# Optimization experiments

Hardware: AMD Instinct MI355X
Metric: run time of the kernel (lower is better)

## Reference

```python
import jax, jax.numpy as jnp
import numpy as np

NEG_INF = -1e30  # safe -inf surrogate to avoid nan in logsumexp


def _ctc_loss_sum(log_probs, labels, input_lengths, label_lengths):
    # log_probs: (T, N, C) already log-softmaxed; blank = 0
    T, N, C = log_probs.shape
    S = labels.shape[1]
    L = 2 * S + 1  # extended label sequence: blank-interleaved

    # extended labels: [blank, y1, blank, y2, ..., blank]
    ext = jnp.zeros((N, L), dtype=jnp.int32).at[:, 1::2].set(labels.astype(jnp.int32))
    # gather emission log-probs for extended labels: (T, N, L)
    lp_ext = jnp.take_along_axis(log_probs, jnp.broadcast_to(ext[None], (T, N, L)), axis=2)

    # transition from l-2 allowed only for non-blank labels differing from ext[l-2]
    ext_m2 = jnp.pad(ext, ((0, 0), (2, 0)), constant_values=-1)[:, :L]
    allow_skip = (ext != 0) & (ext != ext_m2)  # (N, L)

    # alpha at t=0
    alpha0 = jnp.full((N, L), NEG_INF, dtype=log_probs.dtype)
    alpha0 = alpha0.at[:, 0].set(lp_ext[0, :, 0])
    alpha0 = alpha0.at[:, 1].set(jnp.where(label_lengths > 0, lp_ext[0, :, 1], NEG_INF))

    def step(alpha, t_and_lp):
        t, lp_t = t_and_lp  # lp_t: (N, L)
        a1 = jnp.pad(alpha, ((0, 0), (1, 0)), constant_values=NEG_INF)[:, :L]
        a2 = jnp.pad(alpha, ((0, 0), (2, 0)), constant_values=NEG_INF)[:, :L]
        a2 = jnp.where(allow_skip, a2, NEG_INF)
        m = jnp.maximum(jnp.maximum(alpha, a1), a2)
        lse = m + jnp.log(jnp.exp(alpha - m) + jnp.exp(a1 - m) + jnp.exp(a2 - m))
        new = jnp.where(m > NEG_INF / 2, lse + lp_t, NEG_INF)
        # freeze alpha past each sequence's input length
        alpha = jnp.where((t < input_lengths)[:, None], new, alpha)
        return alpha, None

    alpha, _ = jax.lax.scan(step, alpha0, (jnp.arange(1, T), lp_ext[1:]))

    # log-likelihood = logsumexp(alpha[2*Sl], alpha[2*Sl - 1])
    idx = (2 * label_lengths).astype(jnp.int32)
    a_last = jnp.take_along_axis(alpha, idx[:, None], axis=1)[:, 0]
    a_prev = jnp.take_along_axis(alpha, jnp.maximum(idx - 1, 0)[:, None], axis=1)[:, 0]
    a_prev = jnp.where(label_lengths > 0, a_prev, NEG_INF)
    m = jnp.maximum(a_last, a_prev)
    ll = m + jnp.log(jnp.exp(a_last - m) + jnp.exp(a_prev - m))
    loss = -ll
    # zero_infinity=True: replace infinite losses with 0
    loss = jnp.where(loss < -NEG_INF / 2, loss, 0.0)
    return jnp.sum(loss)


def setup_inputs() -> dict:
    T, N, C, S = 512, 32, 4000, 64
    key = jax.random.key(0)
    k1, k2 = jax.random.split(key)
    inputs = jax.random.normal(k1, (T, N, C), dtype=jnp.float32)
    labels = jax.random.randint(k2, (N, S), 1, C, dtype=jnp.int32)  # exclude blank=0
    input_lengths = jnp.full((N,), T, dtype=jnp.int32)
    label_lengths = jnp.full((N,), S, dtype=jnp.int32)
    return {"inputs": inputs, "labels": labels,
            "input_lengths": input_lengths, "label_lengths": label_lengths}


def reference(inputs, labels, input_lengths, label_lengths):
    log_probs = jax.nn.log_softmax(inputs, axis=2)
    return _ctc_loss_sum(log_probs, labels, input_lengths, label_lengths)
```

## Files before the change

kernel.cpp:

```cpp
#include <hip/hip_runtime.h>

#define LN2 0.6931471805599453f

constexpr int T = 512, N = 32, C = 4000, S = 64;
constexpr int TN   = T * N;
constexpr int ROWF = 68;
constexpr int CT   = 16;
constexpr int NC   = T / CT;

__global__ __launch_bounds__(256) void k_softmax_probs(
    const float* __restrict__ x, const int* __restrict__ labels,
    float* __restrict__ pp)
{
    int row  = blockIdx.x * 4 + (threadIdx.x >> 6);
    int lane = threadIdx.x & 63;
    const float*  rp  = x + (size_t)row * C;
    const float4* rp4 = reinterpret_cast<const float4*>(rp);

    float m = -INFINITY, s = 0.f;
    #pragma unroll
    for (int k = 0; k < 15; ++k) {
        float4 v = rp4[lane + 64 * k];
        float mv = fmaxf(fmaxf(v.x, v.y), fmaxf(v.z, v.w));
        float s4 = __expf(v.x - mv) + __expf(v.y - mv) +
                   __expf(v.z - mv) + __expf(v.w - mv);
        float nm = fmaxf(m, mv);
        s = s * __expf(m - nm) + s4 * __expf(mv - nm);
        m = nm;
    }
    if (lane < 40) {
        float4 v = rp4[960 + lane];
        float mv = fmaxf(fmaxf(v.x, v.y), fmaxf(v.z, v.w));
        float s4 = __expf(v.x - mv) + __expf(v.y - mv) +
                   __expf(v.z - mv) + __expf(v.w - mv);
        float nm = fmaxf(m, mv);
        s = s * __expf(m - nm) + s4 * __expf(mv - nm);
        m = nm;
    }
    for (int off = 32; off; off >>= 1) {
        float om = __shfl_xor(m, off), os = __shfl_xor(s, off);
        float nm = fmaxf(m, om);
        s = s * __expf(m - nm) + os * __expf(om - nm);
        m = nm;
    }
    float logZ = m + __logf(s);

    int t = row >> 5, n = row & 31;
    int c = labels[n * S + lane];
    float* outp = pp + ((size_t)n * T + t) * ROWF;
    outp[1 + lane] = __expf(rp[c] - logZ);
    if (lane == 0) outp[0] = __expf(rp[0] - logZ);
}

__device__ __forceinline__ float dpp_shr1_zero(float x) {
    int r = __builtin_amdgcn_update_dpp(0, __float_as_int(x),
                                        0x138 , 0xf, 0xf, false);
    return __int_as_float(r);
}
template <int CTRL>
__device__ __forceinline__ float dpp_max_step(float x) {
    int t = __builtin_amdgcn_update_dpp(__float_as_int(x), __float_as_int(x),
                                        CTRL, 0xf, 0xf, false);
    return fmaxf(x, __int_as_float(t));
}
__device__ __forceinline__ float wave_max_bcast(float x) {
    x = dpp_max_step<0xB1>(x);
    x = dpp_max_step<0x4E>(x);
    x = dpp_max_step<0x141>(x);
    x = dpp_max_step<0x140>(x);
    x = dpp_max_step<0x142>(x);
    x = dpp_max_step<0x143>(x);
    return __int_as_float(__builtin_amdgcn_readlane(__float_as_int(x), 63));
}
__device__ __forceinline__ void renorm_apply(float g, float& a0, float& a1,
                                             float& aX, int& SH, int target) {
    unsigned bits = __float_as_uint(g);
    int k = (bits == 0u) ? 0 : (target - ((int)(bits >> 23) - 127));
    a0 = ldexpf(a0, k); a1 = ldexpf(a1, k); aX = ldexpf(aX, k);
    SH += k;
}

__device__ __forceinline__ void single_step(const float* R, int lane, float skf,
                                            float& a0, float& a1, float& aX) {
    float cb = R[0], cl = R[1 + lane];
    float p1 = dpp_shr1_zero(a1);
    float n0 = (a0 + p1) * cb;
    float n1 = fmaf(skf, p1, a0 + a1) * cl;
    float nX = (aX + a1) * cb;
    a0 = n0; a1 = n1; aX = nX;
}

__device__ __forceinline__ void pair_step(const float* R0, const float* R1,
    int lane, float skf, float skUf, float skk,
    float& a0, float& a1, float& aX)
{
    float cb1 = R0[0], cl1 = R0[1 + lane];
    float cb2 = R1[0], cl2 = R1[1 + lane];
    float clU = dpp_shr1_zero(cl1);
    float W   = clU * cl2;
    float A   = cb1 * cb2;
    float B   = clU * cb2;
    float Cc  = A + B;
    float D   = skUf * B;
    float s1  = cb1 + cl1;
    float E   = s1 * cl2;
    float F   = cl1 * cl2;
    float G   = skf * W;
    float H   = fmaf(skf, F + W, cb1 * cl2);
    float I   = skk * W;
    float Y0  = cl1 * cb2;
    float Y1  = s1 * cb2;
    float Y2  = skf * Y0;
    float p1  = dpp_shr1_zero(a1);
    float p0  = dpp_shr1_zero(a0);
    float p2  = dpp_shr1_zero(p1);
    float n0  = fmaf(p0, B, a0 * A) + fmaf(p2, D, p1 * Cc);
    float n1  = fmaf(a1, F, a0 * E) + fmaf(p2, I, fmaf(p1, H, p0 * G));
    float nX  = fmaf(a1, Y1, aX * A) + fmaf(p1, Y2, a0 * Y0);
    a0 = n0; a1 = n1; aX = nX;
}

__global__ __launch_bounds__(64) void k_ctc_alpha(
    const float* __restrict__ pp, const int* __restrict__ labels,
    const int* __restrict__ input_len, const int* __restrict__ label_len,
    float* __restrict__ loss_out)
{
    __shared__ float lds[2][CT][256];
    const int n = blockIdx.x, lane = threadIdx.x;
    const float* bp = pp + (size_t)n * T * ROWF;
    const int Tin = input_len[n], Sl = label_len[n];

    const int li   = labels[n * S + lane];
    const int lim1 = lane ? labels[n * S + lane - 1] : -1;
    const bool skip_ok = (lane > 0) && (li != 0) && (li != lim1);
    const float skf  = skip_ok ? 1.f : 0.f;
    const float skUf = dpp_shr1_zero(skf);
    const float skk  = skf * skUf;

    asm volatile("s_waitcnt vmcnt(0)" ::: "memory");
    __builtin_amdgcn_sched_barrier(0);

    float a0 = 0.f, a1 = 0.f, aX = 0.f;
    int SH = 0;

#define ISSUE(cc) do {                                                        \
    const float* cp_ = bp + (size_t)(cc) * CT * ROWF;                         \
    _Pragma("unroll")                                                         \
    for (int d_ = 0; d_ < CT; ++d_)                                           \
        __builtin_amdgcn_global_load_lds(cp_ + (size_t)d_ * ROWF + lane * 4,  \
                                         &lds[(cc) & 1][d_][0], 16, 0, 0);    \
    } while (0)

#define WIN4(BUF, D0) do {                                                    \
    float gs_ = fmaxf(fmaxf(a0, a1), aX);                                     \
    pair_step(&lds[BUF][D0    ][0], &lds[BUF][D0 + 1][0], lane, skf, skUf, skk, a0, a1, aX); \
    pair_step(&lds[BUF][D0 + 2][0], &lds[BUF][D0 + 3][0], lane, skf, skUf, skk, a0, a1, aX); \
    pair_step(&lds[BUF][D0 + 4][0], &lds[BUF][D0 + 5][0], lane, skf, skUf, skk, a0, a1, aX); \
    pair_step(&lds[BUF][D0 + 6][0], &lds[BUF][D0 + 7][0], lane, skf, skUf, skk, a0, a1, aX); \
    renorm_apply(wave_max_bcast(gs_), a0, a1, aX, SH, 90);                    \
} while (0)

    ISSUE(0);
    ISSUE(1);

    if (Tin == T) {
        asm volatile("s_waitcnt vmcnt(16)" ::: "memory");
        __builtin_amdgcn_sched_barrier(0);
        a0 = (lane == 0) ? lds[0][0][0] : 0.f;
        a1 = (lane == 0 && Sl > 0) ? lds[0][0][1] : 0.f;
        {
            float gs_ = fmaxf(a0, a1);
            single_step(&lds[0][1][0], lane, skf, a0, a1, aX);
            pair_step(&lds[0][2][0], &lds[0][3][0], lane, skf, skUf, skk, a0, a1, aX);
            pair_step(&lds[0][4][0], &lds[0][5][0], lane, skf, skUf, skk, a0, a1, aX);
            pair_step(&lds[0][6][0], &lds[0][7][0], lane, skf, skUf, skk, a0, a1, aX);
            renorm_apply(wave_max_bcast(gs_), a0, a1, aX, SH, 90);
            WIN4(0, 8);
        }
        __builtin_amdgcn_sched_barrier(0);
        ISSUE(2);
        for (int c = 1; c < NC; ++c) {
            if (c < NC - 1) asm volatile("s_waitcnt vmcnt(16)" ::: "memory");
            else            asm volatile("s_waitcnt vmcnt(0)"  ::: "memory");
            __builtin_amdgcn_sched_barrier(0);
            int buf = c & 1;
            WIN4(buf, 0);
            WIN4(buf, 8);
            if (c + 2 < NC) {
                __builtin_amdgcn_sched_barrier(0);
                ISSUE(c + 2);
            }
        }
    } else {
#define GSTEP(cc, dd) do {                                                    \
    float cb_ = lds[(cc) & 1][dd][0];                                         \
    float cl_ = lds[(cc) & 1][dd][1 + lane];                                  \
    float p1_ = dpp_shr1_zero(a1);                                            \
    float na0_ = (a0 + p1_) * cb_;                                            \
    float na1_ = fmaf(skf, p1_, a0 + a1) * cl_;                               \
    float naX_ = (aX + a1) * cb_;                                             \
    int t_ = (cc) * CT + (dd);                                                \
    bool act_ = (unsigned)(t_ - 1) < (unsigned)(Tin - 1);                     \
    a0 = act_ ? na0_ : a0;                                                    \
    a1 = act_ ? na1_ : a1;                                                    \
    aX = act_ ? naX_ : aX;                                                    \
    if (((dd) & 3) == 3) {                                                    \
        float g_ = wave_max_bcast(fmaxf(a0, fmaxf(a1, aX)));                  \
        renorm_apply(g_, a0, a1, aX, SH, 100);                                \
    }                                                                         \
} while (0)
        asm volatile("s_waitcnt vmcnt(16)" ::: "memory");
        __builtin_amdgcn_sched_barrier(0);
        a0 = (lane == 0) ? lds[0][0][0] : 0.f;
        a1 = (lane == 0 && Sl > 0) ? lds[0][0][1] : 0.f;
        #pragma unroll
        for (int d = 1; d < CT; ++d) GSTEP(0, d);
        __builtin_amdgcn_sched_barrier(0);
        ISSUE(2);
        for (int c = 1; c < NC; ++c) {
            if (c < NC - 1) asm volatile("s_waitcnt vmcnt(16)" ::: "memory");
            else            asm volatile("s_waitcnt vmcnt(0)"  ::: "memory");
            __builtin_amdgcn_sched_barrier(0);
            #pragma unroll
            for (int d = 0; d < CT; ++d) GSTEP(c, d);
            if (c + 2 < NC) {
                __builtin_amdgcn_sched_barrier(0);
                ISSUE(c + 2);
            }
        }
#undef GSTEP
    }
#undef ISSUE
#undef WIN4

    float a_last = (Sl >= S) ? __shfl(aX, 63) : __shfl(a0, Sl);
    float a_prev_raw = __shfl(a1, (Sl > 0) ? (Sl - 1) : 0);
    float a_prev = (Sl > 0) ? a_prev_raw : 0.f;
    if (lane == 0) {
        float sum  = a_last + a_prev;
        float ll2  = log2f(sum) - (float)SH;
        float loss = -ll2 * LN2;
        if (!(loss < 5e29f)) loss = 0.f;
        loss_out[n] = loss;
    }
}

__global__ __launch_bounds__(64) void k_reduce(
    const float* __restrict__ loss, float* __restrict__ out)
{
    int lane = threadIdx.x;
    float v = (lane < N) ? loss[lane] : 0.f;
    for (int off = 32; off; off >>= 1) v += __shfl_xor(v, off);
    if (lane == 0) out[0] = v;
}

extern "C" void kernel_launch(void* const* d_in, const int* in_sizes, int n_in,
                              void* d_out, int out_size, void* d_ws, size_t ws_size,
                              hipStream_t stream) {
    const float* x       = (const float*)d_in[0];
    const int*   labels  = (const int*)d_in[1];
    const int*   in_len  = (const int*)d_in[2];
    const int*   lab_len = (const int*)d_in[3];
    float* out  = (float*)d_out;
    float* pp   = (float*)d_ws;
    float* loss = pp + (size_t)TN * ROWF + 256;

    k_softmax_probs<<<TN / 4, 256, 0, stream>>>(x, labels, pp);
    k_ctc_alpha<<<N, 64, 0, stream>>>(pp, labels, in_len, lab_len, loss);
    k_reduce<<<1, 64, 0, stream>>>(loss, out);
}
```

Before: 90.39 us.

## Prescale emissions per row and pipeline alpha renormalization across windows

The softmax kernel now scales each row's emission probabilities by a per-row power of two and stores the exponents, which the alpha kernel sums and adds back at the end. In the alpha recursion, the wave-wide max reduction for renormalization is spread across the pair steps of the next window, and the scale factor is applied one window late. This takes the serial DPP reduction off the critical dependency chain. It also shrinks the LDS buffer to ROWF and limits global-to-LDS loads to 17 lanes. In exchange it adds an extra workspace array and a delayed-scaling scheme whose headroom must still prevent overflow and underflow.

```diff
diff --git a/kernel.cpp b/kernel.cpp
--- a/kernel.cpp
+++ b/kernel.cpp
@@ -10,7 +10,7 @@
 
 __global__ __launch_bounds__(256) void k_softmax_probs(
     const float* __restrict__ x, const int* __restrict__ labels,
-    float* __restrict__ pp)
+    float* __restrict__ pp, float* __restrict__ ee)
 {
     int row  = blockIdx.x * 4 + (threadIdx.x >> 6);
     int lane = threadIdx.x & 63;
@@ -46,10 +46,22 @@
     float logZ = m + __logf(s);
 
     int t = row >> 5, n = row & 31;
-    int c = labels[n * S + lane];
+    int c  = labels[n * S + lane];
+    float zb = rp[0];
+    float zl = rp[c];
+
+    float wm = zl;
+    for (int off = 32; off; off >>= 1) wm = fmaxf(wm, __shfl_xor(wm, off));
+    wm = fmaxf(wm, zb);
+    float pm = __expf(wm - logZ);
+    int e = (int)(__float_as_uint(pm) >> 23) - 127;
+
     float* outp = pp + ((size_t)n * T + t) * ROWF;
-    outp[1 + lane] = __expf(rp[c] - logZ);
-    if (lane == 0) outp[0] = __expf(rp[0] - logZ);
+    outp[1 + lane] = ldexpf(__expf(zl - logZ), -e);
+    if (lane == 0) {
+        outp[0] = ldexpf(__expf(zb - logZ), -e);
+        ee[n * T + t] = (float)e;
+    }
 }
 
 __device__ __forceinline__ float dpp_shr1_zero(float x) {
@@ -72,68 +84,21 @@
     x = dpp_max_step<0x143>(x);
     return __int_as_float(__builtin_amdgcn_readlane(__float_as_int(x), 63));
 }
-__device__ __forceinline__ void renorm_apply(float g, float& a0, float& a1,
-                                             float& aX, int& SH, int target) {
-    unsigned bits = __float_as_uint(g);
-    int k = (bits == 0u) ? 0 : (target - ((int)(bits >> 23) - 127));
-    a0 = ldexpf(a0, k); a1 = ldexpf(a1, k); aX = ldexpf(aX, k);
-    SH += k;
-}
-
-__device__ __forceinline__ void single_step(const float* R, int lane, float skf,
-                                            float& a0, float& a1, float& aX) {
-    float cb = R[0], cl = R[1 + lane];
-    float p1 = dpp_shr1_zero(a1);
-    float n0 = (a0 + p1) * cb;
-    float n1 = fmaf(skf, p1, a0 + a1) * cl;
-    float nX = (aX + a1) * cb;
-    a0 = n0; a1 = n1; aX = nX;
-}
-
-__device__ __forceinline__ void pair_step(const float* R0, const float* R1,
-    int lane, float skf, float skUf, float skk,
-    float& a0, float& a1, float& aX)
-{
-    float cb1 = R0[0], cl1 = R0[1 + lane];
-    float cb2 = R1[0], cl2 = R1[1 + lane];
-    float clU = dpp_shr1_zero(cl1);
-    float W   = clU * cl2;
-    float A   = cb1 * cb2;
-    float B   = clU * cb2;
-    float Cc  = A + B;
-    float D   = skUf * B;
-    float s1  = cb1 + cl1;
-    float E   = s1 * cl2;
-    float F   = cl1 * cl2;
-    float G   = skf * W;
-    float H   = fmaf(skf, F + W, cb1 * cl2);
-    float I   = skk * W;
-    float Y0  = cl1 * cb2;
-    float Y1  = s1 * cb2;
-    float Y2  = skf * Y0;
-    float p1  = dpp_shr1_zero(a1);
-    float p0  = dpp_shr1_zero(a0);
-    float p2  = dpp_shr1_zero(p1);
-    float n0  = fmaf(p0, B, a0 * A) + fmaf(p2, D, p1 * Cc);
-    float n1  = fmaf(a1, F, a0 * E) + fmaf(p2, I, fmaf(p1, H, p0 * G));
-    float nX  = fmaf(a1, Y1, aX * A) + fmaf(p1, Y2, a0 * Y0);
-    a0 = n0; a1 = n1; aX = nX;
-}
 
 __global__ __launch_bounds__(64) void k_ctc_alpha(
-    const float* __restrict__ pp, const int* __restrict__ labels,
+    const float* __restrict__ pp, const float* __restrict__ ee,
+    const int* __restrict__ labels,
     const int* __restrict__ input_len, const int* __restrict__ label_len,
     float* __restrict__ loss_out)
 {
-    __shared__ float lds[2][CT][256];
+    __shared__ __align__(16) float lds[2][CT][ROWF];
     const int n = blockIdx.x, lane = threadIdx.x;
+    const int Tin = input_len[n], Sl = label_len[n];
     const float* bp = pp + (size_t)n * T * ROWF;
-    const int Tin = input_len[n], Sl = label_len[n];
 
     const int li   = labels[n * S + lane];
     const int lim1 = lane ? labels[n * S + lane - 1] : -1;
-    const bool skip_ok = (lane > 0) && (li != 0) && (li != lim1);
-    const float skf  = skip_ok ? 1.f : 0.f;
+    const float skf  = (lane > 0 && li != 0 && li != lim1) ? 1.f : 0.f;
     const float skUf = dpp_shr1_zero(skf);
     const float skk  = skf * skUf;
 
@@ -141,51 +106,98 @@
     __builtin_amdgcn_sched_barrier(0);
 
     float a0 = 0.f, a1 = 0.f, aX = 0.f;
-    int SH = 0;
+    int SH = 0, kA = 0;
+    float gs = 0.f;
 
 #define ISSUE(cc) do {                                                        \
     const float* cp_ = bp + (size_t)(cc) * CT * ROWF;                         \
-    _Pragma("unroll")                                                         \
-    for (int d_ = 0; d_ < CT; ++d_)                                           \
-        __builtin_amdgcn_global_load_lds(cp_ + (size_t)d_ * ROWF + lane * 4,  \
-                                         &lds[(cc) & 1][d_][0], 16, 0, 0);    \
-    } while (0)
-
-#define WIN4(BUF, D0) do {                                                    \
-    float gs_ = fmaxf(fmaxf(a0, a1), aX);                                     \
-    pair_step(&lds[BUF][D0    ][0], &lds[BUF][D0 + 1][0], lane, skf, skUf, skk, a0, a1, aX); \
-    pair_step(&lds[BUF][D0 + 2][0], &lds[BUF][D0 + 3][0], lane, skf, skUf, skk, a0, a1, aX); \
-    pair_step(&lds[BUF][D0 + 4][0], &lds[BUF][D0 + 5][0], lane, skf, skUf, skk, a0, a1, aX); \
-    pair_step(&lds[BUF][D0 + 6][0], &lds[BUF][D0 + 7][0], lane, skf, skUf, skk, a0, a1, aX); \
-    renorm_apply(wave_max_bcast(gs_), a0, a1, aX, SH, 90);                    \
+    if (lane < 17) {                                                          \
+        _Pragma("unroll")                                                     \
+        for (int d_ = 0; d_ < CT; ++d_)                                       \
+            __builtin_amdgcn_global_load_lds(cp_ + (size_t)d_ * ROWF + lane * 4, \
+                                             &lds[(cc) & 1][d_][0], 16, 0, 0);\
+    } } while (0)
+
+#define PAIRS(B, D) do {                                                      \
+    const float* R0_ = &lds[B][D][0];                                         \
+    const float* R1_ = &lds[B][(D) + 1][0];                                   \
+    float cb1 = R0_[0], cl1 = R0_[1 + lane];                                  \
+    float cb2 = R1_[0], cl2 = R1_[1 + lane];                                  \
+    float clU = dpp_shr1_zero(cl1);                                           \
+    float W   = clU * cl2;                                                    \
+    float A   = cb1 * cb2;                                                    \
+    float B_  = clU * cb2;                                                    \
+    float Cc  = A + B_;                                                       \
+    float D_  = skUf * B_;                                                    \
+    float s1  = cb1 + cl1;                                                    \
+    float E   = s1 * cl2;                                                     \
+    float F   = cl1 * cl2;                                                    \
+    float G   = skf * W;                                                      \
+    float H   = fmaf(skf, F + W, cb1 * cl2);                                  \
+    float I   = skk * W;                                                      \
+    float Y0  = cl1 * cb2;                                                    \
+    float Y1  = s1 * cb2;                                                     \
+    float Y2  = skf * Y0;                                                     \
+    float p1  = dpp_shr1_zero(a1);                                            \
+    float p0  = dpp_shr1_zero(a0);                                            \
+    float p2  = dpp_shr1_zero(p1);                                            \
+    float n0  = fmaf(p0, B_, a0 * A) + fmaf(p2, D_, p1 * Cc);                 \
+    float n1  = fmaf(a1, F, a0 * E) + fmaf(p2, I, fmaf(p1, H, p0 * G));       \
+    float nX  = fmaf(a1, Y1, aX * A) + fmaf(p1, Y2, a0 * Y0);                 \
+    a0 = n0; a1 = n1; aX = nX;                                                \
 } while (0)
 
-    ISSUE(0);
-    ISSUE(1);
+#define WINDOW4(B, D0) do {                                                   \
+    a0 = ldexpf(a0, kA); a1 = ldexpf(a1, kA); aX = ldexpf(aX, kA);            \
+    SH += kA;                                                                 \
+    float gnow_ = fmaxf(fmaxf(a0, a1), aX);                                   \
+    PAIRS(B, D0);                                                             \
+    gs = dpp_max_step<0xB1>(gs);  gs = dpp_max_step<0x4E>(gs);                \
+    PAIRS(B, (D0) + 2);                                                       \
+    gs = dpp_max_step<0x141>(gs); gs = dpp_max_step<0x140>(gs);               \
+    PAIRS(B, (D0) + 4);                                                       \
+    gs = dpp_max_step<0x142>(gs); gs = dpp_max_step<0x143>(gs);               \
+    PAIRS(B, (D0) + 6);                                                       \
+    {   unsigned b_ = (unsigned)__builtin_amdgcn_readlane(__float_as_int(gs), 63); \
+        int e_ = (int)(b_ >> 23) - 127;                                       \
+        kA = (b_ == 0u) ? 0 : (105 - e_ - kA);                                \
+    }                                                                         \
+    gs = gnow_;                                                               \
+} while (0)
 
     if (Tin == T) {
+        ISSUE(0); ISSUE(1);
         asm volatile("s_waitcnt vmcnt(16)" ::: "memory");
         __builtin_amdgcn_sched_barrier(0);
         a0 = (lane == 0) ? lds[0][0][0] : 0.f;
         a1 = (lane == 0 && Sl > 0) ? lds[0][0][1] : 0.f;
         {
-            float gs_ = fmaxf(a0, a1);
-            single_step(&lds[0][1][0], lane, skf, a0, a1, aX);
-            pair_step(&lds[0][2][0], &lds[0][3][0], lane, skf, skUf, skk, a0, a1, aX);
-            pair_step(&lds[0][4][0], &lds[0][5][0], lane, skf, skUf, skk, a0, a1, aX);
-            pair_step(&lds[0][6][0], &lds[0][7][0], lane, skf, skUf, skk, a0, a1, aX);
-            renorm_apply(wave_max_bcast(gs_), a0, a1, aX, SH, 90);
-            WIN4(0, 8);
-        }
+            float cb = lds[0][1][0], cl = lds[0][1][1 + lane];
+            float p1 = dpp_shr1_zero(a1);
+            float n0 = (a0 + p1) * cb;
+            float n1 = fmaf(skf, p1, a0 + a1) * cl;
+            float nX = (aX + a1) * cb;
+            a0 = n0; a1 = n1; aX = nX;
+        }
+        PAIRS(0, 2); PAIRS(0, 4); PAIRS(0, 6);
+        {
+            float g = wave_max_bcast(fmaxf(fmaxf(a0, a1), aX));
+            unsigned b = __float_as_uint(g);
+            int k0 = (b == 0u) ? 0 : (105 - ((int)(b >> 23) - 127));
+            a0 = ldexpf(a0, k0); a1 = ldexpf(a1, k0); aX = ldexpf(aX, k0);
+            SH += k0; kA = 0;
+            gs = fmaxf(fmaxf(a0, a1), aX);
+        }
+        WINDOW4(0, 8);
         __builtin_amdgcn_sched_barrier(0);
         ISSUE(2);
         for (int c = 1; c < NC; ++c) {
-            if (c < NC - 1) asm volatile("s_waitcnt vmcnt(16)" ::: "memory");
-            else            asm volatile("s_waitcnt vmcnt(0)"  ::: "memory");
+            if (c < NC - 1) { asm volatile("s_waitcnt vmcnt(16)" ::: "memory"); }
+            else            { asm volatile("s_waitcnt vmcnt(0)"  ::: "memory"); }
             __builtin_amdgcn_sched_barrier(0);
             int buf = c & 1;
-            WIN4(buf, 0);
-            WIN4(buf, 8);
+            WINDOW4(buf, 0);
+            WINDOW4(buf, 8);
             if (c + 2 < NC) {
                 __builtin_amdgcn_sched_barrier(0);
                 ISSUE(c + 2);
@@ -206,9 +218,13 @@
     aX = act_ ? naX_ : aX;                                                    \
     if (((dd) & 3) == 3) {                                                    \
         float g_ = wave_max_bcast(fmaxf(a0, fmaxf(a1, aX)));                  \
-        renorm_apply(g_, a0, a1, aX, SH, 100);                                \
+        unsigned b_ = __float_as_uint(g_);                                    \
+        int k_ = (b_ == 0u) ? 0 : (100 - ((int)(b_ >> 23) - 127));            \
+        a0 = ldexpf(a0, k_); a1 = ldexpf(a1, k_); aX = ldexpf(aX, k_);        \
+        SH += k_;                                                             \
     }                                                                         \
 } while (0)
+        ISSUE(0); ISSUE(1);
         asm volatile("s_waitcnt vmcnt(16)" ::: "memory");
         __builtin_amdgcn_sched_barrier(0);
         a0 = (lane == 0) ? lds[0][0][0] : 0.f;
@@ -218,8 +234,8 @@
         __builtin_amdgcn_sched_barrier(0);
         ISSUE(2);
         for (int c = 1; c < NC; ++c) {
-            if (c < NC - 1) asm volatile("s_waitcnt vmcnt(16)" ::: "memory");
-            else            asm volatile("s_waitcnt vmcnt(0)"  ::: "memory");
+            if (c < NC - 1) { asm volatile("s_waitcnt vmcnt(16)" ::: "memory"); }
+            else            { asm volatile("s_waitcnt vmcnt(0)"  ::: "memory"); }
             __builtin_amdgcn_sched_barrier(0);
             #pragma unroll
             for (int d = 0; d < CT; ++d) GSTEP(c, d);
@@ -230,15 +246,25 @@
         }
 #undef GSTEP
     }
+#undef WINDOW4
+#undef PAIRS
 #undef ISSUE
-#undef WIN4
+
+    float se = 0.f;
+    #pragma unroll
+    for (int j = 0; j < 8; ++j) {
+        int idx = lane + 64 * j;
+        float ev = ee[n * T + idx];
+        se += (idx < Tin) ? ev : 0.f;
+    }
+    for (int off = 32; off; off >>= 1) se += __shfl_xor(se, off);
 
     float a_last = (Sl >= S) ? __shfl(aX, 63) : __shfl(a0, Sl);
     float a_prev_raw = __shfl(a1, (Sl > 0) ? (Sl - 1) : 0);
     float a_prev = (Sl > 0) ? a_prev_raw : 0.f;
     if (lane == 0) {
         float sum  = a_last + a_prev;
-        float ll2  = log2f(sum) - (float)SH;
+        float ll2  = log2f(sum) - (float)SH + se;
         float loss = -ll2 * LN2;
         if (!(loss < 5e29f)) loss = 0.f;
         loss_out[n] = loss;
@@ -263,9 +289,10 @@
     const int*   lab_len = (const int*)d_in[3];
     float* out  = (float*)d_out;
     float* pp   = (float*)d_ws;
-    float* loss = pp + (size_t)TN * ROWF + 256;
-
-    k_softmax_probs<<<TN / 4, 256, 0, stream>>>(x, labels, pp);
-    k_ctc_alpha<<<N, 64, 0, stream>>>(pp, labels, in_len, lab_len, loss);
+    float* ee   = pp + (size_t)TN * ROWF + 256;
+    float* loss = ee + TN;
+
+    k_softmax_probs<<<TN / 4, 256, 0, stream>>>(x, labels, pp, ee);
+    k_ctc_alpha<<<N, 64, 0, stream>>>(pp, ee, labels, in_len, lab_len, loss);
     k_reduce<<<1, 64, 0, stream>>>(loss, out);
 }
```

Measured after the change: 92.64 us. +2.5%, slower.
